# Optimization experiments

Hardware: AMD Instinct MI355X
Metric: run time of the kernel (lower is better)

Reference implementation:

```python
import jax, jax.numpy as jnp
import numpy as np

D_MODEL, D_K, D_V, H = 1024, 64, 64, 16
B, N = 4, 2048


def setup_inputs() -> dict:
    key = jax.random.key(0)
    ks = jax.random.split(key, 11)
    s = 0.02
    return {
        "Q": jax.random.normal(ks[0], (B, N, D_MODEL), jnp.float32),
        "K": jax.random.normal(ks[1], (B, N, D_MODEL), jnp.float32),
        "V": jax.random.normal(ks[2], (B, N, D_MODEL), jnp.float32),
        # stacked per-head projection weights: [h, d_model, d_k]
        "Wq": jax.random.normal(ks[3], (H, D_MODEL, D_K), jnp.float32) * s,
        "bq": jax.random.normal(ks[4], (H, D_K), jnp.float32) * s,
        "Wk": jax.random.normal(ks[5], (H, D_MODEL, D_K), jnp.float32) * s,
        "bk": jax.random.normal(ks[6], (H, D_K), jnp.float32) * s,
        "Wv": jax.random.normal(ks[7], (H, D_MODEL, D_V), jnp.float32) * s,
        "bv": jax.random.normal(ks[8], (H, D_V), jnp.float32) * s,
        "Wo": jax.random.normal(ks[9], (H * D_V, D_MODEL), jnp.float32) * s,
        "bo": jax.random.normal(ks[10], (D_MODEL,), jnp.float32) * s,
        "apply_mask": 1,
    }


def reference(Q, K, V, Wq, bq, Wk, bk, Wv, bv, Wo, bo, apply_mask):
    # fused per-head projections: [b, h, n, d_k]
    q = jnp.einsum("bnd,hdk->bhnk", Q, Wq) + bq[None, :, None, :]
    k = jnp.einsum("bnd,hdk->bhnk", K, Wk) + bk[None, :, None, :]
    v = jnp.einsum("bnd,hdv->bhnv", V, Wv) + bv[None, :, None, :]
    scores = jnp.einsum("bhnk,bhmk->bhnm", q, k) / jnp.sqrt(
        jnp.asarray(D_K, q.dtype)
    )
    if apply_mask:
        n = Q.shape[1]
        causal = jnp.tril(jnp.ones((n, n), dtype=bool))
        scores = jnp.where(causal[None, None], scores, -jnp.inf)
    weights = jax.nn.softmax(scores, axis=-1)
    out = jnp.einsum("bhnm,bhmv->bhnv", weights, v)
    # concat heads: [b, n, h*d_v]
    out = out.transpose(0, 2, 1, 3).reshape(Q.shape[0], Q.shape[1], H * D_V)
    return out @ Wo + bo
```

## Files before the change

kernel.cpp:

```cpp
#include <hip/hip_runtime.h>
#include <hip/hip_bf16.h>

#define H 16
#define DM 1024
#define DK 64
#define B_ 4
#define N_ 2048

typedef __attribute__((ext_vector_type(8))) short bf16x8;
typedef __attribute__((ext_vector_type(4))) short s16x4;
typedef __attribute__((ext_vector_type(2))) unsigned int u32x2;
typedef __attribute__((ext_vector_type(4))) float f32x4;

static __device__ __forceinline__ short f2bs(float x) {
    __hip_bfloat16 b = __float2bfloat16(x);
    return *reinterpret_cast<short*>(&b);
}

static __device__ __forceinline__ void async16(const void* g, void* l) {
    __builtin_amdgcn_global_load_lds(
        (const __attribute__((address_space(1))) void*)g,
        (__attribute__((address_space(3))) void*)l, 16, 0, 0);
}

static __device__ __forceinline__ unsigned packbf(float lo, float hi) {
    return __builtin_amdgcn_perm(__float_as_uint(hi), __float_as_uint(lo), 0x07060302u);
}

__global__ __launch_bounds__(256) void prep_kernel(
    const float* __restrict__ Q, const float* __restrict__ K, const float* __restrict__ V,
    const float* __restrict__ Wq, const float* __restrict__ Wk,
    const float* __restrict__ Wv, const float* __restrict__ Wo,
    short* __restrict__ Qb, short* __restrict__ Kb, short* __restrict__ Vb,
    short* __restrict__ wqT, short* __restrict__ wkT,
    short* __restrict__ wvT, short* __restrict__ woT)
{
    int y = blockIdx.y;
    if (y < 3) {
        const float* s = (y == 0) ? Q : (y == 1) ? K : V;
        short* d = (y == 0) ? Qb : (y == 1) ? Kb : Vb;
        size_t i = ((size_t)blockIdx.x * 256 + threadIdx.x) * 8;
        f32x4 a = *(const f32x4*)(s + i);
        f32x4 b = *(const f32x4*)(s + i + 4);
        bf16x8 p;
        #pragma unroll
        for (int j = 0; j < 4; ++j) { p[j] = f2bs(a[j]); p[4 + j] = f2bs(b[j]); }
        *(bf16x8*)(d + i) = p;
        return;
    }
    if (blockIdx.x >= 1024) return;
    __shared__ float tile[64][65];
    int z = blockIdx.x >> 8;
    int bx = blockIdx.x & 255;
    int t = threadIdx.x;
    int tj = t & 63, ti = t >> 6;

    if (z < 3) {
        const float* src = (z == 0) ? Wq : (z == 1) ? Wk : Wv;
        short* dst = (z == 0) ? wqT : (z == 1) ? wkT : wvT;
        int h = bx >> 4;
        int dmt = bx & 15;
        #pragma unroll
        for (int r = 0; r < 16; ++r) {
            int i = r * 4 + ti;
            tile[i][tj] = src[((size_t)h * 1024 + dmt * 64 + i) * 64 + tj];
        }
        __syncthreads();
        #pragma unroll
        for (int r = 0; r < 16; ++r) {
            int dk = r * 4 + ti;
            dst[((size_t)h * 64 + dk) * 1024 + dmt * 64 + tj] = f2bs(tile[tj][dk]);
        }
    } else {
        int kt = bx >> 4;
        int nt = bx & 15;
        #pragma unroll
        for (int r = 0; r < 16; ++r) {
            int i = r * 4 + ti;
            tile[i][tj] = Wo[((size_t)kt * 64 + i) * 1024 + nt * 64 + tj];
        }
        __syncthreads();
        #pragma unroll
        for (int r = 0; r < 16; ++r) {
            int jn = r * 4 + ti;
            woT[((size_t)nt * 64 + jn) * 1024 + kt * 64 + tj] = f2bs(tile[tj][jn]);
        }
    }
}

static __device__ __forceinline__ void gemm_mainloop(
    const short* __restrict__ A, const short* __restrict__ BT,
    int rowM0, int colN0, char* lds, f32x4 (&acc)[4][4])
{
    int tid = threadIdx.x;
    int lane = tid & 63, w = tid >> 6;
    int l16 = lane & 15, quad = lane >> 4;
    int wm = w >> 1, wn = w & 1;
    int xg = (quad ^ ((l16 >> 1) & 3)) << 4;

    int r0 = w * 32 + (lane >> 2);
    int gsl = ((lane & 3) ^ ((lane >> 3) & 3)) << 4;
    int dst0 = w * 2048 + lane * 16;
    const char* Ag0 = (const char*)A + (size_t)(rowM0 + r0) * 2048 + gsl;
    const char* Ag1 = Ag0 + 16 * 2048;
    const char* Bg0 = (const char*)BT + (size_t)(colN0 + r0) * 2048 + gsl;
    const char* Bg1 = Bg0 + 16 * 2048;

    #pragma unroll
    for (int t = 0; t < 3; ++t) {
        size_t kb = (size_t)t * 64;
        char* As = lds + t * 16384;
        char* Bs = As + 8192;
        async16(Ag0 + kb, As + dst0);
        async16(Ag1 + kb, As + dst0 + 1024);
        async16(Bg0 + kb, Bs + dst0);
        async16(Bg1 + kb, Bs + dst0 + 1024);
    }

    int c0 = 0;
    for (int it = 0; it < 32; ++it) {
        if (it < 30)       asm volatile("s_waitcnt vmcnt(8)" ::: "memory");
        else if (it == 30) asm volatile("s_waitcnt vmcnt(4)" ::: "memory");
        else               asm volatile("s_waitcnt vmcnt(0)" ::: "memory");
        __builtin_amdgcn_s_barrier();
        asm volatile("" ::: "memory");
        __builtin_amdgcn_sched_barrier(0);

        const char* As = lds + c0;
        const char* Bs = As + 8192;
        bf16x8 a[4], b[4];
        #pragma unroll
        for (int i = 0; i < 4; ++i)
            a[i] = *(const bf16x8*)(As + (wm * 64 + i * 16 + l16) * 64 + xg);
        #pragma unroll
        for (int j = 0; j < 4; ++j)
            b[j] = *(const bf16x8*)(Bs + (wn * 64 + j * 16 + l16) * 64 + xg);
        #pragma unroll
        for (int i = 0; i < 4; ++i)
            #pragma unroll
            for (int j = 0; j < 4; ++j)
                acc[i][j] = __builtin_amdgcn_mfma_f32_16x16x32_bf16(a[i], b[j], acc[i][j], 0, 0, 0);

        asm volatile("" ::: "memory");
        __builtin_amdgcn_s_barrier();
        __builtin_amdgcn_sched_barrier(0);
        if (it + 3 < 32) {
            size_t kb = (size_t)(it + 3) * 64;
            char* Aw = lds + c0;
            char* Bw = Aw + 8192;
            async16(Ag0 + kb, Aw + dst0);
            async16(Ag1 + kb, Aw + dst0 + 1024);
            async16(Bg0 + kb, Bw + dst0);
            async16(Bg1 + kb, Bw + dst0 + 1024);
        }
        c0 += 16384;
        if (c0 == 49152) c0 = 0;
    }
}

__global__ __launch_bounds__(256) void proj_gemm(
    const short* __restrict__ Qb, const short* __restrict__ Kb, const short* __restrict__ Vb,
    const short* __restrict__ wqT, const short* __restrict__ wkT, const short* __restrict__ wvT,
    const float* __restrict__ bq, const float* __restrict__ bk, const float* __restrict__ bv,
    short* __restrict__ qbuf, short* __restrict__ kbuf, short* __restrict__ vTbuf)
{
    __shared__ char lds[49152];
    int which = blockIdx.z;
    const short* A  = (which == 0) ? Qb : (which == 1) ? Kb : Vb;
    const short* BT = (which == 0) ? wqT : (which == 1) ? wkT : wvT;
    const float* bias = (which == 0) ? bq : (which == 1) ? bk : bv;

    int rowM0 = blockIdx.x * 128;
    int colN0 = blockIdx.y * 128;

    f32x4 acc[4][4];
    #pragma unroll
    for (int i = 0; i < 4; ++i)
        #pragma unroll
        for (int j = 0; j < 4; ++j) acc[i][j] = (f32x4){0.f, 0.f, 0.f, 0.f};

    gemm_mainloop(A, BT, rowM0, colN0, lds, acc);

    int lane = threadIdx.x & 63, w = threadIdx.x >> 6;
    int l16 = lane & 15, quad = lane >> 4;
    int wm = w >> 1, wn = w & 1;

    if (which == 2) {
        #pragma unroll
        for (int j = 0; j < 4; ++j) {
            int col = colN0 + wn * 64 + j * 16 + l16;
            int hh = col >> 6, dv = col & 63;
            float bs = bias[col];
            #pragma unroll
            for (int i = 0; i < 4; ++i) {
                int rowb = rowM0 + wm * 64 + i * 16 + quad * 4;
                int bb = rowb >> 11, n0 = rowb & 2047;
                s16x4 pk;
                #pragma unroll
                for (int r = 0; r < 4; ++r) pk[r] = f2bs(acc[i][j][r] + bs);
                *(s16x4*)(vTbuf + (((size_t)bb * H + hh) * DK + dv) * N_ + n0) = pk;
            }
        }
    } else {
        short* dst = (which == 0) ? qbuf : kbuf;
        float scl = (which == 0) ? 0.180336880f : 1.0f;
        #pragma unroll
        for (int j = 0; j < 4; ++j) {
            int col = colN0 + wn * 64 + j * 16 + l16;
            float bs = bias[col];
            #pragma unroll
            for (int i = 0; i < 4; ++i) {
                int rowb = rowM0 + wm * 64 + i * 16 + quad * 4;
                #pragma unroll
                for (int r = 0; r < 4; ++r)
                    dst[(size_t)(rowb + r) * 1024 + col] = f2bs((acc[i][j][r] + bs) * scl);
            }
        }
    }
}

__global__ __launch_bounds__(256) void out_gemm(
    const short* __restrict__ obuf, const short* __restrict__ woT,
    const float* __restrict__ bo, float* __restrict__ out)
{
    __shared__ char lds[49152];
    int rowM0 = blockIdx.x * 128;
    int colN0 = blockIdx.y * 128;

    f32x4 acc[4][4];
    #pragma unroll
    for (int i = 0; i < 4; ++i)
        #pragma unroll
        for (int j = 0; j < 4; ++j) acc[i][j] = (f32x4){0.f, 0.f, 0.f, 0.f};

    gemm_mainloop(obuf, woT, rowM0, colN0, lds, acc);

    int lane = threadIdx.x & 63, w = threadIdx.x >> 6;
    int l16 = lane & 15, quad = lane >> 4;
    int wm = w >> 1, wn = w & 1;

    #pragma unroll
    for (int j = 0; j < 4; ++j) {
        int col = colN0 + wn * 64 + j * 16 + l16;
        float bs = bo[col];
        #pragma unroll
        for (int i = 0; i < 4; ++i) {
            int rowb = rowM0 + wm * 64 + i * 16 + quad * 4;
            #pragma unroll
            for (int r = 0; r < 4; ++r)
                out[(size_t)(rowb + r) * 1024 + col] = acc[i][j][r] + bs;
        }
    }
}

__global__ __launch_bounds__(256) void flash_kernel(
    const short* __restrict__ qbuf, const short* __restrict__ kbuf, const short* __restrict__ vT,
    short* __restrict__ obuf, const int* __restrict__ amask)
{
    __shared__ short Ks[2][4096];
    __shared__ short Vs[2][4096];
    __shared__ char  plds[4][2048];

    int bid = blockIdx.x;
    int g = bid & 7, idx = bid >> 3;
    int bh = g * 8 + (idx >> 4);
    int xq = idx & 15;
    int b = bh >> 4, h = bh & 15;

    int tid = threadIdx.x;
    int lane = tid & 63, wave = tid >> 6;
    int l16 = lane & 15, quad = lane >> 4;
    int msk = amask[0];

    int i8 = lane >> 3, i7 = lane & 7;
    int sg = (i7 ^ i8) << 4;
    int pk0 = i8 * 4 + wave;
    int skey = wave * 16 + i8;
    int ldst = wave * 2048 + lane * 16;

    const char* kbase = (const char*)(kbuf + (size_t)b * 2048 * 1024 + h * 64);
    const char* vbase = (const char*)(vT + ((size_t)(b * 16 + h) * 64) * 2048);

    int m7 = l16 & 7;
    int g0 = (quad ^ m7) << 4;
    int g1 = ((4 | quad) ^ m7) << 4;

    char* pw = plds[wave];
    int prd0 = l16 * 128 + g0;
    int prd1 = l16 * 128 + g1;
    int pwa[4];
    #pragma unroll
    for (int r = 0; r < 4; ++r) {
        int row = quad * 4 + r;
        pwa[r] = row * 128 + (((l16 >> 1) ^ (row & 7)) << 4) + ((l16 & 1) << 3);
    }

    for (int pass = 0; pass < 2; ++pass) {
        int qt = pass ? (31 - xq) : xq;
        int qw = qt * 64 + wave * 16;
        int nkb = msk ? (qt + 1) : 32;

        const short* qp = qbuf + ((size_t)(b * 2048 + qw + l16)) * 1024 + h * 64;
        bf16x8 aq0 = *(const bf16x8*)(qp + quad * 8);
        bf16x8 aq1 = *(const bf16x8*)(qp + 32 + quad * 8);

        f32x4 o[4];
        float lsum[4];
        #pragma unroll
        for (int i = 0; i < 4; ++i) { o[i] = (f32x4){0.f, 0.f, 0.f, 0.f}; lsum[i] = 0.f; }

        async16(kbase + (size_t)pk0 * 2048 + sg, (char*)Ks[0] + ldst);
        async16(kbase + (size_t)(pk0 + 32) * 2048 + sg, (char*)Ks[0] + ldst + 1024);
        async16(vbase + (size_t)skey * 4096 + sg, (char*)Vs[0] + ldst);
        async16(vbase + (size_t)(skey + 8) * 4096 + sg, (char*)Vs[0] + ldst + 1024);

        for (int ib = 0; ib < nkb; ++ib) {
            __syncthreads();
            int cur = ib & 1;
            if (ib + 1 < nkb) {
                int nb = (ib + 1) & 1;
                size_t kb2 = (size_t)(ib + 1) * 64;
                async16(kbase + (kb2 + pk0) * 2048 + sg, (char*)Ks[nb] + ldst);
                async16(kbase + (kb2 + pk0 + 32) * 2048 + sg, (char*)Ks[nb] + ldst + 1024);
                async16(vbase + (size_t)skey * 4096 + kb2 * 2 + sg, (char*)Vs[nb] + ldst);
                async16(vbase + (size_t)(skey + 8) * 4096 + kb2 * 2 + sg, (char*)Vs[nb] + ldst + 1024);
            }
            int kb = ib * 64;

            f32x4 s[4];
            __builtin_amdgcn_s_setprio(1);
            #pragma unroll
            for (int nt = 0; nt < 4; ++nt) {
                const char* kr = (const char*)Ks[cur] + (nt * 16 + l16) * 128;
                bf16x8 b0 = *(const bf16x8*)(kr + g0);
                bf16x8 b1 = *(const bf16x8*)(kr + g1);
                f32x4 t = (f32x4){0.f, 0.f, 0.f, 0.f};
                t = __builtin_amdgcn_mfma_f32_16x16x32_bf16(aq0, b0, t, 0, 0, 0);
                t = __builtin_amdgcn_mfma_f32_16x16x32_bf16(aq1, b1, t, 0, 0, 0);
                s[nt] = t;
            }
            __builtin_amdgcn_s_setprio(0);

            if (msk && (kb + 63 > qw)) {
                #pragma unroll
                for (int r = 0; r < 4; ++r) {
                    int row = qw + quad * 4 + r;
                    #pragma unroll
                    for (int nt = 0; nt < 4; ++nt) {
                        int col = kb + l16 * 4 + nt;
                        if (col > row) s[nt][r] = -3e38f;
                    }
                }
            }

            __builtin_amdgcn_wave_barrier();
            #pragma unroll
            for (int r = 0; r < 4; ++r) {
                float p0 = __builtin_amdgcn_exp2f(s[0][r]);
                float p1 = __builtin_amdgcn_exp2f(s[1][r]);
                float p2 = __builtin_amdgcn_exp2f(s[2][r]);
                float p3 = __builtin_amdgcn_exp2f(s[3][r]);
                lsum[r] += (p0 + p1) + (p2 + p3);
                u32x2 pk;
                pk[0] = packbf(p0, p1);
                pk[1] = packbf(p2, p3);
                *(u32x2*)(pw + pwa[r]) = pk;
            }
            __builtin_amdgcn_wave_barrier();
            bf16x8 ap0 = *(const bf16x8*)(pw + prd0);
            bf16x8 ap1 = *(const bf16x8*)(pw + prd1);
            __builtin_amdgcn_wave_barrier();

            __builtin_amdgcn_s_setprio(1);
            #pragma unroll
            for (int vb = 0; vb < 4; ++vb) {
                const char* vr = (const char*)Vs[cur] + (vb * 16 + l16) * 128;
                bf16x8 v0 = *(const bf16x8*)(vr + g0);
                bf16x8 v1 = *(const bf16x8*)(vr + g1);
                o[vb] = __builtin_amdgcn_mfma_f32_16x16x32_bf16(ap0, v0, o[vb], 0, 0, 0);
                o[vb] = __builtin_amdgcn_mfma_f32_16x16x32_bf16(ap1, v1, o[vb], 0, 0, 0);
            }
            __builtin_amdgcn_s_setprio(0);
        }

        #pragma unroll
        for (int r = 0; r < 4; ++r) {
            float t = lsum[r];
            #pragma unroll
            for (int off = 1; off < 16; off <<= 1) t += __shfl_xor(t, off, 64);
            float inv = 1.0f / t;
            int row = qw + quad * 4 + r;
            #pragma unroll
            for (int vb = 0; vb < 4; ++vb)
                obuf[((size_t)(b * 2048 + row)) * 1024 + h * 64 + vb * 16 + l16] =
                    f2bs(o[vb][r] * inv);
        }
        __syncthreads();
    }
}

extern "C" void kernel_launch(void* const* d_in, const int* in_sizes, int n_in,
                              void* d_out, int out_size, void* d_ws, size_t ws_size,
                              hipStream_t stream)
{
    const float* Q  = (const float*)d_in[0];
    const float* K  = (const float*)d_in[1];
    const float* V  = (const float*)d_in[2];
    const float* Wq = (const float*)d_in[3];
    const float* bq = (const float*)d_in[4];
    const float* Wk = (const float*)d_in[5];
    const float* bk = (const float*)d_in[6];
    const float* Wv = (const float*)d_in[7];
    const float* bv = (const float*)d_in[8];
    const float* Wo = (const float*)d_in[9];
    const float* bo = (const float*)d_in[10];
    const int* amask = (const int*)d_in[11];
    float* out = (float*)d_out;

    char* ws = (char*)d_ws;
    const size_t SZ = (size_t)B_ * N_ * DM * sizeof(short);
    const size_t SZW = (size_t)H * DK * DM * sizeof(short);
    short* Qb    = (short*)ws; ws += SZ;
    short* Kb    = (short*)ws; ws += SZ;
    short* Vb    = (short*)ws; ws += SZ;
    short* qbuf  = (short*)ws; ws += SZ;
    short* kbuf  = (short*)ws; ws += SZ;
    short* vTbuf = (short*)ws; ws += SZ;
    short* wqT   = (short*)ws; ws += SZW;
    short* wkT   = (short*)ws; ws += SZW;
    short* wvT   = (short*)ws; ws += SZW;
    short* woT   = (short*)ws; ws += SZW;
    short* obuf  = Qb;

    prep_kernel<<<dim3(4096, 4), dim3(256), 0, stream>>>(Q, K, V, Wq, Wk, Wv, Wo,
                                                         Qb, Kb, Vb, wqT, wkT, wvT, woT);
    proj_gemm<<<dim3(64, 8, 3), dim3(256), 0, stream>>>(Qb, Kb, Vb, wqT, wkT, wvT,
                                                        bq, bk, bv, qbuf, kbuf, vTbuf);
    flash_kernel<<<dim3(1024), dim3(256), 0, stream>>>(qbuf, kbuf, vTbuf, obuf, amask);
    out_gemm<<<dim3(64, 8), dim3(256), 0, stream>>>(obuf, woT, bo, out);
}
```

Before: 310.3 us.

## Restructure GEMM pipeline to single barrier per step and add XCD-aware tile swizzle

The GEMM mainloop now issues the next-but-one stage's async global-to-LDS loads right after a single barrier, before the MFMA compute on the current stage. This removes the second barrier per iteration, at the cost of prefetching two stages ahead instead of three. Both projection and output GEMMs switch to a 1D grid with a block-to-tile remapping. The remapping groups row tiles that run on the same XCD, aiming to improve L2 reuse of shared A/B tiles. The prefetch depth is reduced, which may expose more load latency.

```diff
diff --git a/kernel.cpp b/kernel.cpp
--- a/kernel.cpp
+++ b/kernel.cpp
@@ -107,7 +107,7 @@
     const char* Bg1 = Bg0 + 16 * 2048;
 
     #pragma unroll
-    for (int t = 0; t < 3; ++t) {
+    for (int t = 0; t < 2; ++t) {
         size_t kb = (size_t)t * 64;
         char* As = lds + t * 16384;
         char* Bs = As + 8192;
@@ -118,43 +118,41 @@
     }
 
     int c0 = 0;
+    int cr = 32768;
     for (int it = 0; it < 32; ++it) {
-        if (it < 30)       asm volatile("s_waitcnt vmcnt(8)" ::: "memory");
-        else if (it == 30) asm volatile("s_waitcnt vmcnt(4)" ::: "memory");
-        else               asm volatile("s_waitcnt vmcnt(0)" ::: "memory");
-        __builtin_amdgcn_s_barrier();
-        asm volatile("" ::: "memory");
-        __builtin_amdgcn_sched_barrier(0);
-
-        const char* As = lds + c0;
-        const char* Bs = As + 8192;
-        bf16x8 a[4], b[4];
-        #pragma unroll
-        for (int i = 0; i < 4; ++i)
-            a[i] = *(const bf16x8*)(As + (wm * 64 + i * 16 + l16) * 64 + xg);
-        #pragma unroll
-        for (int j = 0; j < 4; ++j)
-            b[j] = *(const bf16x8*)(Bs + (wn * 64 + j * 16 + l16) * 64 + xg);
-        #pragma unroll
-        for (int i = 0; i < 4; ++i)
-            #pragma unroll
-            for (int j = 0; j < 4; ++j)
-                acc[i][j] = __builtin_amdgcn_mfma_f32_16x16x32_bf16(a[i], b[j], acc[i][j], 0, 0, 0);
-
-        asm volatile("" ::: "memory");
+        if (it < 31) asm volatile("s_waitcnt vmcnt(4)" ::: "memory");
+        else         asm volatile("s_waitcnt vmcnt(0)" ::: "memory");
         __builtin_amdgcn_s_barrier();
         __builtin_amdgcn_sched_barrier(0);
-        if (it + 3 < 32) {
-            size_t kb = (size_t)(it + 3) * 64;
-            char* Aw = lds + c0;
+
+        if (it + 2 < 32) {
+            size_t kb = (size_t)(it + 2) * 64;
+            char* Aw = lds + cr;
             char* Bw = Aw + 8192;
             async16(Ag0 + kb, Aw + dst0);
             async16(Ag1 + kb, Aw + dst0 + 1024);
             async16(Bg0 + kb, Bw + dst0);
             async16(Bg1 + kb, Bw + dst0 + 1024);
         }
-        c0 += 16384;
-        if (c0 == 49152) c0 = 0;
+        __builtin_amdgcn_sched_barrier(0);
+
+        const char* As = lds + c0;
+        const char* Bs = As + 8192;
+        bf16x8 a[4], b[4];
+        #pragma unroll
+        for (int i = 0; i < 4; ++i)
+            a[i] = *(const bf16x8*)(As + (wm * 64 + i * 16 + l16) * 64 + xg);
+        #pragma unroll
+        for (int j = 0; j < 4; ++j)
+            b[j] = *(const bf16x8*)(Bs + (wn * 64 + j * 16 + l16) * 64 + xg);
+        #pragma unroll
+        for (int i = 0; i < 4; ++i)
+            #pragma unroll
+            for (int j = 0; j < 4; ++j)
+                acc[i][j] = __builtin_amdgcn_mfma_f32_16x16x32_bf16(a[i], b[j], acc[i][j], 0, 0, 0);
+
+        c0 += 16384; if (c0 == 49152) c0 = 0;
+        cr += 16384; if (cr == 49152) cr = 0;
     }
 }
 
@@ -165,13 +163,20 @@
     short* __restrict__ qbuf, short* __restrict__ kbuf, short* __restrict__ vTbuf)
 {
     __shared__ char lds[49152];
-    int which = blockIdx.z;
+    int id = blockIdx.x;
+    int xcd = id & 7;
+    int k = id >> 3;
+    int which = k >> 6;
+    int rem = k & 63;
+    int r = ((rem >> 3) << 3) | xcd;
+    int c = rem & 7;
+
     const short* A  = (which == 0) ? Qb : (which == 1) ? Kb : Vb;
     const short* BT = (which == 0) ? wqT : (which == 1) ? wkT : wvT;
     const float* bias = (which == 0) ? bq : (which == 1) ? bk : bv;
 
-    int rowM0 = blockIdx.x * 128;
-    int colN0 = blockIdx.y * 128;
+    int rowM0 = r * 128;
+    int colN0 = c * 128;
 
     f32x4 acc[4][4];
     #pragma unroll
@@ -197,7 +202,7 @@
                 int bb = rowb >> 11, n0 = rowb & 2047;
                 s16x4 pk;
                 #pragma unroll
-                for (int r = 0; r < 4; ++r) pk[r] = f2bs(acc[i][j][r] + bs);
+                for (int r2 = 0; r2 < 4; ++r2) pk[r2] = f2bs(acc[i][j][r2] + bs);
                 *(s16x4*)(vTbuf + (((size_t)bb * H + hh) * DK + dv) * N_ + n0) = pk;
             }
         }
@@ -212,8 +217,8 @@
             for (int i = 0; i < 4; ++i) {
                 int rowb = rowM0 + wm * 64 + i * 16 + quad * 4;
                 #pragma unroll
-                for (int r = 0; r < 4; ++r)
-                    dst[(size_t)(rowb + r) * 1024 + col] = f2bs((acc[i][j][r] + bs) * scl);
+                for (int r2 = 0; r2 < 4; ++r2)
+                    dst[(size_t)(rowb + r2) * 1024 + col] = f2bs((acc[i][j][r2] + bs) * scl);
             }
         }
     }
@@ -224,8 +229,14 @@
     const float* __restrict__ bo, float* __restrict__ out)
 {
     __shared__ char lds[49152];
-    int rowM0 = blockIdx.x * 128;
-    int colN0 = blockIdx.y * 128;
+    int id = blockIdx.x;
+    int xcd = id & 7;
+    int k = id >> 3;
+    int r = ((k >> 3) << 3) | xcd;
+    int c = k & 7;
+
+    int rowM0 = r * 128;
+    int colN0 = c * 128;
 
     f32x4 acc[4][4];
     #pragma unroll
@@ -247,8 +258,8 @@
         for (int i = 0; i < 4; ++i) {
             int rowb = rowM0 + wm * 64 + i * 16 + quad * 4;
             #pragma unroll
-            for (int r = 0; r < 4; ++r)
-                out[(size_t)(rowb + r) * 1024 + col] = acc[i][j][r] + bs;
+            for (int r2 = 0; r2 < 4; ++r2)
+                out[(size_t)(rowb + r2) * 1024 + col] = acc[i][j][r2] + bs;
         }
     }
 }
@@ -434,8 +445,8 @@
 
     prep_kernel<<<dim3(4096, 4), dim3(256), 0, stream>>>(Q, K, V, Wq, Wk, Wv, Wo,
                                                          Qb, Kb, Vb, wqT, wkT, wvT, woT);
-    proj_gemm<<<dim3(64, 8, 3), dim3(256), 0, stream>>>(Qb, Kb, Vb, wqT, wkT, wvT,
-                                                        bq, bk, bv, qbuf, kbuf, vTbuf);
+    proj_gemm<<<dim3(1536), dim3(256), 0, stream>>>(Qb, Kb, Vb, wqT, wkT, wvT,
+                                                    bq, bk, bv, qbuf, kbuf, vTbuf);
     flash_kernel<<<dim3(1024), dim3(256), 0, stream>>>(qbuf, kbuf, vTbuf, obuf, amask);
-    out_gemm<<<dim3(64, 8), dim3(256), 0, stream>>>(obuf, woT, bo, out);
-}
+    out_gemm<<<dim3(512), dim3(256), 0, stream>>>(obuf, woT, bo, out);
+}
```

Result: faster. 303.3 us (-2.3%).
